# Performance work log

Measured on AMD Instinct MI355X. Metric: run time of the kernel, lower is better.

Reference implementation:

```python
import jax, jax.numpy as jnp
import numpy as np

M = 16          # num_particles
EPS = 0.006


def setup_inputs() -> dict:
    key = jax.random.key(0)
    k1, k2, k3, k4 = jax.random.split(key, 4)
    B, P, O = 131072, 16, 4  # batch, pred_horizon, obs_horizon
    return {
        "ys_t": jax.random.normal(k1, (B, P, O), dtype=jnp.float32),
        "ys_r_stop": jax.random.normal(k2, (B, P, O), dtype=jnp.float32),
        "w_scale": jax.random.uniform(k3, (B,), dtype=jnp.float32),
        "time_weights": jax.random.uniform(k4, (B,), dtype=jnp.float32),
    }


def _laplace(a, b, ws, D):
    # a,b: [G, M, D]; ws: [G, M] (scale indexed by j, the first particle index)
    d = jnp.linalg.norm(a[:, :, None, :] - b[:, None, :, :], axis=-1)  # [G, M, M]
    d = jnp.maximum(d, EPS)
    return jnp.exp(-ws[:, :, None] * d / D)


def reference(ys_t, ys_r_stop, w_scale, time_weights):
    B = ys_t.shape[0]
    G = B // M
    x = ys_t.reshape(G, M, -1)        # [G, M, D]
    y = ys_r_stop.reshape(G, M, -1)   # [G, M, D]
    D = x.shape[-1]                   # pred_horizon * obs_horizon (dim_normalize)
    ws = w_scale.reshape(G, M)
    tw = time_weights.reshape(G, M)[:, 0]  # [G]
    terms = _laplace(x, x, ws, D) + _laplace(y, y, ws, D) - 2.0 * _laplace(x, y, ws, D)
    group_loss = terms.sum(axis=(1, 2)) * tw / (M * M)  # [G]
    return group_loss.sum() / G
```

## Files before the change

kernel.cpp:

```cpp
#include <hip/hip_runtime.h>


#define EPS_D 0.006f
#define L2E_D64 0.022542110013890053f
#define EXP2(x) __builtin_amdgcn_exp2f(x)

#define ROT(v, O) __int_as_float(__builtin_amdgcn_update_dpp(              \
        0, __float_as_int(v), 0x120 + (O), 0xF, 0xF, false))

#define SWZ(v, PAT) __int_as_float(__builtin_amdgcn_ds_swizzle(            \
        __float_as_int(v), PAT))
#define XOR16(v) SWZ(v, 0x401F)
#define XOR8(v)  SWZ(v, 0x201F)
#define XOR4(v)  SWZ(v, 0x101F)
#define XOR2(v)  SWZ(v, 0x081F)
#define XOR1(v)  SWZ(v, 0x041F)

__global__ __launch_bounds__(256, 6)
void imm_loss_kernel(const float* __restrict__ ys_t,
                     const float* __restrict__ ys_r,
                     const float* __restrict__ w_scale,
                     const float* __restrict__ time_w,
                     float* __restrict__ partials)
{
    const int tid  = threadIdx.x;
    const int lane = tid & 63;
    const int wave = tid >> 6;
    const int g    = blockIdx.x * 4 + wave;
    const int j    = lane & 15;
    const int db   = lane >> 4;

    __shared__ float4 lds4[4][256];
    __shared__ float smem[4];

    const float4* xg = reinterpret_cast<const float4*>(ys_t + (size_t)g * 1024);
    const float4* yg = reinterpret_cast<const float4*>(ys_r + (size_t)g * 1024);

    const float s_j = w_scale[g * 16 + j] * L2E_D64;
    const float tw  = time_w[g * 16];

    {
        float4 xs[4];
        #pragma unroll
        for (int k = 0; k < 4; ++k) {
            const int r  = 4 * k + db;
            const int gq = j ^ (r & 7);
            xs[k] = xg[r * 16 + gq];
        }
        #pragma unroll
        for (int k = 0; k < 4; ++k) lds4[wave][k * 64 + lane] = xs[k];
    }

    float xarr[16];
    #pragma unroll
    for (int m = 0; m < 4; ++m) {
        const int sl = (db * 4 + m) ^ (j & 7);
        const float4 v = lds4[wave][j * 16 + sl];
        xarr[4*m+0] = v.x; xarr[4*m+1] = v.y; xarr[4*m+2] = v.z; xarr[4*m+3] = v.w;
    }

    {
        float4 yv[4];
        #pragma unroll
        for (int k = 0; k < 4; ++k) {
            const int r  = 4 * k + db;
            const int gq = j ^ (r & 7);
            yv[k] = yg[r * 16 + gq];
        }
        #pragma unroll
        for (int k = 0; k < 4; ++k) lds4[wave][k * 64 + lane] = yv[k];
    }

    float nx = 0.f, ny = 0.f, g0 = 0.f;
    float gxx[8], gyy[8], gxy[8], hxy[7];
    #pragma unroll
    for (int i = 0; i < 8; ++i) { gxx[i] = 0.f; gyy[i] = 0.f; gxy[i] = 0.f; }
    #pragma unroll
    for (int i = 0; i < 7; ++i) hxy[i] = 0.f;

#define ACC_FULL(O) {                                                      \
            const float xr = ROT(xd, O);                                   \
            const float yr = ROT(yd, O);                                   \
            gxx[(O)-1] = fmaf(xr, xd, gxx[(O)-1]);                         \
            gyy[(O)-1] = fmaf(yr, yd, gyy[(O)-1]);                         \
            gxy[(O)-1] = fmaf(yr, xd, gxy[(O)-1]); }
#define ACC_XY(O) {                                                        \
            const float yr = ROT(yd, O);                                   \
            hxy[(O)-9] = fmaf(yr, xd, hxy[(O)-9]); }

#define GRAM4(M) {                                                         \
        const int sl = (db * 4 + (M)) ^ (j & 7);                           \
        const float4 wv = lds4[wave][j * 16 + sl];                         \
        _Pragma("unroll")                                                  \
        for (int e = 0; e < 4; ++e) {                                      \
            const float xd = xarr[4*(M)+e];                                \
            const float yd = (e == 0) ? wv.x : (e == 1) ? wv.y             \
                           : (e == 2) ? wv.z : wv.w;                       \
            nx = fmaf(xd, xd, nx);                                         \
            ny = fmaf(yd, yd, ny);                                         \
            g0 = fmaf(xd, yd, g0);                                         \
            ACC_FULL(1) ACC_FULL(2) ACC_FULL(3) ACC_FULL(4)                \
            ACC_FULL(5) ACC_FULL(6) ACC_FULL(7) ACC_FULL(8)                \
            ACC_XY(9)  ACC_XY(10) ACC_XY(11) ACC_XY(12)                    \
            ACC_XY(13) ACC_XY(14) ACC_XY(15)                               \
        } }

    GRAM4(0)
    GRAM4(1)
    GRAM4(2)
    GRAM4(3)

#define RED(v) { v += XOR16(v); v += __shfl_xor(v, 32, 64); }
    RED(nx) RED(ny) RED(g0)
    #pragma unroll
    for (int i = 0; i < 8; ++i) { RED(gxx[i]) RED(gyy[i]) RED(gxy[i]) }
    #pragma unroll
    for (int i = 0; i < 7; ++i) { RED(hxy[i]) }

    float acc = 2.0f * EXP2(-s_j * EPS_D);

    {
        const float d2 = fmaxf(nx + ny - 2.0f * g0, 0.0f);
        const float dd = fmaxf(sqrtf(d2), EPS_D);
        acc -= 2.0f * EXP2(-s_j * dd);
    }

#define FIN_FULL(O, W) {                                                   \
        const float sk  = ROT(s_j, O);                                     \
        const float nxr = ROT(nx, O);                                      \
        const float nyr = ROT(ny, O);                                      \
        const float ddx = fmaxf(sqrtf(fmaxf(nx + nxr - 2.0f*gxx[(O)-1], 0.f)), EPS_D); \
        const float ddy = fmaxf(sqrtf(fmaxf(ny + nyr - 2.0f*gyy[(O)-1], 0.f)), EPS_D); \
        const float ddz = fmaxf(sqrtf(fmaxf(nx + nyr - 2.0f*gxy[(O)-1], 0.f)), EPS_D); \
        acc += (W) * (EXP2(-s_j * ddx) + EXP2(-sk * ddx));                 \
        acc += (W) * (EXP2(-s_j * ddy) + EXP2(-sk * ddy));                 \
        acc -= 2.0f * EXP2(-s_j * ddz); }

#define FIN_XY(O) {                                                        \
        const float nyr = ROT(ny, O);                                      \
        const float ddz = fmaxf(sqrtf(fmaxf(nx + nyr - 2.0f*hxy[(O)-9], 0.f)), EPS_D); \
        acc -= 2.0f * EXP2(-s_j * ddz); }

    FIN_FULL(1, 1.0f)
    FIN_FULL(2, 1.0f)
    FIN_FULL(3, 1.0f)
    FIN_FULL(4, 1.0f)
    FIN_FULL(5, 1.0f)
    FIN_FULL(6, 1.0f)
    FIN_FULL(7, 1.0f)
    FIN_FULL(8, 0.5f)
    FIN_XY(9)
    FIN_XY(10)
    FIN_XY(11)
    FIN_XY(12)
    FIN_XY(13)
    FIN_XY(14)
    FIN_XY(15)

    float val = acc * tw;
    val += __shfl_xor(val, 32, 64);
    val += XOR16(val);
    val += XOR8(val);
    val += XOR4(val);
    val += XOR2(val);
    val += XOR1(val);

    if (lane == 0) smem[wave] = val;
    __syncthreads();
    if (tid == 0)
        partials[blockIdx.x] = smem[0] + smem[1] + smem[2] + smem[3];
}

__global__ void imm_reduce_kernel(const float* __restrict__ part, int n,
                                  float inv_scale, float* __restrict__ out)
{
    const int tid = threadIdx.x;
    float v = 0.f;
    for (int i = tid; i < n; i += 256) v += part[i];
    #pragma unroll
    for (int off = 32; off; off >>= 1) v += __shfl_xor(v, off, 64);
    __shared__ float s[4];
    if ((tid & 63) == 0) s[tid >> 6] = v;
    __syncthreads();
    if (tid == 0) out[0] = (s[0] + s[1] + s[2] + s[3]) * inv_scale;
}

extern "C" void kernel_launch(void* const* d_in, const int* in_sizes, int n_in,
                              void* d_out, int out_size, void* d_ws, size_t ws_size,
                              hipStream_t stream)
{
    const float* ys_t = (const float*)d_in[0];
    const float* ys_r = (const float*)d_in[1];
    const float* wsc  = (const float*)d_in[2];
    const float* twp  = (const float*)d_in[3];
    float* out      = (float*)d_out;
    float* partials = (float*)d_ws;

    const int B = in_sizes[2];
    const int G = B / 16;
    const int blocks = G / 4;

    imm_loss_kernel<<<blocks, 256, 0, stream>>>(ys_t, ys_r, wsc, twp, partials);

    const float inv_scale = 1.0f / (1024.0f * (float)G);
    imm_reduce_kernel<<<1, 256, 0, stream>>>(partials, blocks, inv_scale, out);
}
```

Baseline: 119.3 us.

## Reuse x rotations for cross terms and split finalization across lane groups

The cross-term Gram accumulation now reuses the already rotated x value (xr·yd) for offsets 1–7, replacing the separate offsets 9–15 that each needed an extra DPP rotation of y. The finalization, which every one of the four replicated lane groups (db) used to compute in full, is now partitioned: each db group evaluates a disjoint subset of rotation offsets, and the final scale factor changes from 1/1024 to 1/256 to match. This targets redundant DPP moves and redundant exp/sqrt work. Because the db split is a divergent branch inside one wavefront, the four branches may run serially, which could cancel much of the finalization saving.

```diff
diff --git a/kernel.cpp b/kernel.cpp
--- a/kernel.cpp
+++ b/kernel.cpp
@@ -72,21 +72,25 @@
     }
 
     float nx = 0.f, ny = 0.f, g0 = 0.f;
-    float gxx[8], gyy[8], gxy[8], hxy[7];
+    float gxx[8], gyy[8], gxy[8], hxy2[7];
     #pragma unroll
     for (int i = 0; i < 8; ++i) { gxx[i] = 0.f; gyy[i] = 0.f; gxy[i] = 0.f; }
     #pragma unroll
-    for (int i = 0; i < 7; ++i) hxy[i] = 0.f;
-
-#define ACC_FULL(O) {                                                      \
+    for (int i = 0; i < 7; ++i) hxy2[i] = 0.f;
+
+#define ACC_FULLX(O) {                                                     \
             const float xr = ROT(xd, O);                                   \
             const float yr = ROT(yd, O);                                   \
-            gxx[(O)-1] = fmaf(xr, xd, gxx[(O)-1]);                         \
-            gyy[(O)-1] = fmaf(yr, yd, gyy[(O)-1]);                         \
-            gxy[(O)-1] = fmaf(yr, xd, gxy[(O)-1]); }
-#define ACC_XY(O) {                                                        \
-            const float yr = ROT(yd, O);                                   \
-            hxy[(O)-9] = fmaf(yr, xd, hxy[(O)-9]); }
+            gxx[(O)-1]  = fmaf(xr, xd, gxx[(O)-1]);                        \
+            gyy[(O)-1]  = fmaf(yr, yd, gyy[(O)-1]);                        \
+            gxy[(O)-1]  = fmaf(yr, xd, gxy[(O)-1]);                        \
+            hxy2[(O)-1] = fmaf(xr, yd, hxy2[(O)-1]); }
+#define ACC_FULL8 {                                                        \
+            const float xr = ROT(xd, 8);                                   \
+            const float yr = ROT(yd, 8);                                   \
+            gxx[7] = fmaf(xr, xd, gxx[7]);                                 \
+            gyy[7] = fmaf(yr, yd, gyy[7]);                                 \
+            gxy[7] = fmaf(yr, xd, gxy[7]); }
 
 #define GRAM4(M) {                                                         \
         const int sl = (db * 4 + (M)) ^ (j & 7);                           \
@@ -99,10 +103,8 @@
             nx = fmaf(xd, xd, nx);                                         \
             ny = fmaf(yd, yd, ny);                                         \
             g0 = fmaf(xd, yd, g0);                                         \
-            ACC_FULL(1) ACC_FULL(2) ACC_FULL(3) ACC_FULL(4)                \
-            ACC_FULL(5) ACC_FULL(6) ACC_FULL(7) ACC_FULL(8)                \
-            ACC_XY(9)  ACC_XY(10) ACC_XY(11) ACC_XY(12)                    \
-            ACC_XY(13) ACC_XY(14) ACC_XY(15)                               \
+            ACC_FULLX(1) ACC_FULLX(2) ACC_FULLX(3) ACC_FULLX(4)            \
+            ACC_FULLX(5) ACC_FULLX(6) ACC_FULLX(7) ACC_FULL8               \
         } }
 
     GRAM4(0)
@@ -115,47 +117,45 @@
     #pragma unroll
     for (int i = 0; i < 8; ++i) { RED(gxx[i]) RED(gyy[i]) RED(gxy[i]) }
     #pragma unroll
-    for (int i = 0; i < 7; ++i) { RED(hxy[i]) }
-
-    float acc = 2.0f * EXP2(-s_j * EPS_D);
-
-    {
-        const float d2 = fmaxf(nx + ny - 2.0f * g0, 0.0f);
-        const float dd = fmaxf(sqrtf(d2), EPS_D);
-        acc -= 2.0f * EXP2(-s_j * dd);
-    }
-
-#define FIN_FULL(O, W) {                                                   \
+    for (int i = 0; i < 7; ++i) { RED(hxy2[i]) }
+
+    float acc = 0.0f;
+
+#define FIN_PAIR(O) {                                                      \
         const float sk  = ROT(s_j, O);                                     \
         const float nxr = ROT(nx, O);                                      \
         const float nyr = ROT(ny, O);                                      \
         const float ddx = fmaxf(sqrtf(fmaxf(nx + nxr - 2.0f*gxx[(O)-1], 0.f)), EPS_D); \
         const float ddy = fmaxf(sqrtf(fmaxf(ny + nyr - 2.0f*gyy[(O)-1], 0.f)), EPS_D); \
         const float ddz = fmaxf(sqrtf(fmaxf(nx + nyr - 2.0f*gxy[(O)-1], 0.f)), EPS_D); \
-        acc += (W) * (EXP2(-s_j * ddx) + EXP2(-sk * ddx));                 \
-        acc += (W) * (EXP2(-s_j * ddy) + EXP2(-sk * ddy));                 \
+        const float ddw = fmaxf(sqrtf(fmaxf(nxr + ny - 2.0f*hxy2[(O)-1], 0.f)), EPS_D); \
+        acc += EXP2(-s_j * ddx) + EXP2(-sk * ddx);                         \
+        acc += EXP2(-s_j * ddy) + EXP2(-sk * ddy);                         \
+        acc -= 2.0f * EXP2(-s_j * ddz);                                    \
+        acc -= 2.0f * EXP2(-sk  * ddw); }
+
+#define FIN_F8 {                                                           \
+        const float sk  = ROT(s_j, 8);                                     \
+        const float nxr = ROT(nx, 8);                                      \
+        const float nyr = ROT(ny, 8);                                      \
+        const float ddx = fmaxf(sqrtf(fmaxf(nx + nxr - 2.0f*gxx[7], 0.f)), EPS_D); \
+        const float ddy = fmaxf(sqrtf(fmaxf(ny + nyr - 2.0f*gyy[7], 0.f)), EPS_D); \
+        const float ddz = fmaxf(sqrtf(fmaxf(nx + nyr - 2.0f*gxy[7], 0.f)), EPS_D); \
+        acc += 0.5f * (EXP2(-s_j * ddx) + EXP2(-sk * ddx));                \
+        acc += 0.5f * (EXP2(-s_j * ddy) + EXP2(-sk * ddy));                \
         acc -= 2.0f * EXP2(-s_j * ddz); }
 
-#define FIN_XY(O) {                                                        \
-        const float nyr = ROT(ny, O);                                      \
-        const float ddz = fmaxf(sqrtf(fmaxf(nx + nyr - 2.0f*hxy[(O)-9], 0.f)), EPS_D); \
-        acc -= 2.0f * EXP2(-s_j * ddz); }
-
-    FIN_FULL(1, 1.0f)
-    FIN_FULL(2, 1.0f)
-    FIN_FULL(3, 1.0f)
-    FIN_FULL(4, 1.0f)
-    FIN_FULL(5, 1.0f)
-    FIN_FULL(6, 1.0f)
-    FIN_FULL(7, 1.0f)
-    FIN_FULL(8, 0.5f)
-    FIN_XY(9)
-    FIN_XY(10)
-    FIN_XY(11)
-    FIN_XY(12)
-    FIN_XY(13)
-    FIN_XY(14)
-    FIN_XY(15)
+    if (db == 0)      { FIN_PAIR(1) FIN_PAIR(5) }
+    else if (db == 1) { FIN_PAIR(2) FIN_PAIR(6) }
+    else if (db == 2) { FIN_PAIR(3) FIN_PAIR(7) }
+    else {
+        FIN_PAIR(4)
+        FIN_F8
+        acc += 2.0f * EXP2(-s_j * EPS_D);
+        const float d2 = fmaxf(nx + ny - 2.0f * g0, 0.0f);
+        const float dd = fmaxf(sqrtf(d2), EPS_D);
+        acc -= 2.0f * EXP2(-s_j * dd);
+    }
 
     float val = acc * tw;
     val += __shfl_xor(val, 32, 64);
@@ -202,6 +202,6 @@
 
     imm_loss_kernel<<<blocks, 256, 0, stream>>>(ys_t, ys_r, wsc, twp, partials);
 
-    const float inv_scale = 1.0f / (1024.0f * (float)G);
+    const float inv_scale = 1.0f / (256.0f * (float)G);
     imm_reduce_kernel<<<1, 256, 0, stream>>>(partials, blocks, inv_scale, out);
 }
```

Result: slower. 145.8 us (+22.2%).
